# Kernel optimization log

Measured on AMD Instinct MI355X. Metric: run time of the kernel, lower is better.

The kernel has to match this reference:

```python
import jax, jax.numpy as jnp
import numpy as np

NI = 2048           # per-node feature dim
H = 2 * NI          # flattened per-sample GRU state (2 nodes)
BS = 4096
NO = 1
NUM_ROUNDS = 2


def setup_inputs() -> dict:
    key = jax.random.key(0)
    ks = jax.random.split(key, 8)
    s_ih = 1.0 / np.sqrt(H)
    features = jax.random.normal(ks[0], (BS, 2, NI), dtype=jnp.float32)
    # torch.nn.GRUCell(H, H): weight_ih [3H, H], weight_hh [3H, H], biases [3H]
    W_ih = jax.random.uniform(ks[1], (3 * H, H), minval=-s_ih, maxval=s_ih, dtype=jnp.float32)
    b_ih = jax.random.uniform(ks[2], (3 * H,), minval=-s_ih, maxval=s_ih, dtype=jnp.float32)
    W_hh = jax.random.uniform(ks[3], (3 * H, H), minval=-s_ih, maxval=s_ih, dtype=jnp.float32)
    b_hh = jax.random.uniform(ks[4], (3 * H,), minval=-s_ih, maxval=s_ih, dtype=jnp.float32)
    # fc = nn.Linear(2*ni, no)
    fc_w = jax.random.uniform(ks[5], (NO, H), minval=-s_ih, maxval=s_ih, dtype=jnp.float32)
    fc_b = jax.random.uniform(ks[6], (NO,), minval=-s_ih, maxval=s_ih, dtype=jnp.float32)
    return {"features": features, "W_ih": W_ih, "b_ih": b_ih,
            "W_hh": W_hh, "b_hh": b_hh, "fc_w": fc_w, "fc_b": fc_b}


def _gru_cell(x, h, W_ih, b_ih, W_hh, b_hh):
    # torch GRUCell semantics
    gi = x @ W_ih.T + b_ih              # [bs, 3H]
    gh = h @ W_hh.T + b_hh              # [bs, 3H]
    i_r, i_z, i_n = jnp.split(gi, 3, axis=-1)
    h_r, h_z, h_n = jnp.split(gh, 3, axis=-1)
    r = jax.nn.sigmoid(i_r + h_r)
    z = jax.nn.sigmoid(i_z + h_z)
    n = jnp.tanh(i_n + r * h_n)
    return (1.0 - z) * n + z * h


def reference(features, W_ih, b_ih, W_hh, b_hh, fc_w, fc_b):
    bs = features.shape[0]
    ni = features.shape[2]
    h = features.reshape(bs, -1)        # [bs, 2*ni] = node0 || node1
    for _ in range(NUM_ROUNDS):
        # fully-connected 2-node graph, sum-aggregate of neighbor messages:
        # node0 receives h1, node1 receives h0 -> x is the half-swap of h
        x = jnp.concatenate([h[:, ni:], h[:, :ni]], axis=-1)
        h = _gru_cell(x, h, W_ih, b_ih, W_hh, b_hh)
    return h @ fc_w.T + fc_b            # [bs, no]
```

## Files before the change

### kernel.cpp

```cpp
#include <hip/hip_runtime.h>


typedef __bf16 bf16x8 __attribute__((ext_vector_type(8)));
typedef float  f32x4  __attribute__((ext_vector_type(4)));
typedef unsigned short u16x4 __attribute__((ext_vector_type(4)));

#define HH    4096
#define NI_D  2048
#define N3H   12288
#define N6H   24576
#define BSZ   4096
#define BM    256
#define BN    256
#define BK    64
#define MT    (BSZ / BM)
#define NT    (N6H / BN)
#define GRID_GEMM (MT * NT)
#define NKT   (HH / BK)

__device__ __forceinline__ unsigned short f2bf(float f) {
  unsigned u = __float_as_uint(f);
  u += 0x7FFFu + ((u >> 16) & 1u);
  return (unsigned short)(u >> 16);
}
__device__ __forceinline__ float bf2f(unsigned short s) {
  return __uint_as_float(((unsigned)s) << 16);
}

__device__ __forceinline__ void gload16(const void* g, void* l) {
  void* gv = (void*)g;
  __builtin_amdgcn_global_load_lds(
      (__attribute__((address_space(1))) unsigned int*)gv,
      (__attribute__((address_space(3))) unsigned int*)l,
      16, 0, 0);
}

__global__ void __launch_bounds__(256)
convert_weights(const float* __restrict__ Wih, const float* __restrict__ Whh,
                unsigned short* __restrict__ Wc)
{
  int idx = (blockIdx.x * 256 + threadIdx.x) << 2;
  int j = idx >> 12;
  int k = idx & 4095;
  const float* src;
  if (j < N3H) src = Wih + (size_t)j * HH + ((k + NI_D) & (HH - 1));
  else         src = Whh + (size_t)(j - N3H) * HH + k;
  f32x4 v = *(const f32x4*)src;
  u16x4 o = { f2bf(v[0]), f2bf(v[1]), f2bf(v[2]), f2bf(v[3]) };
  *(u16x4*)(Wc + idx) = o;
}

__global__ void __launch_bounds__(256)
cast_f32_bf16(const float* __restrict__ src, unsigned short* __restrict__ dst)
{
  int i = (blockIdx.x * 256 + threadIdx.x) << 2;
  f32x4 v = *(const f32x4*)(src + i);
  u16x4 o = { f2bf(v[0]), f2bf(v[1]), f2bf(v[2]), f2bf(v[3]) };
  *(u16x4*)(dst + i) = o;
}

__global__ void __launch_bounds__(512, 2)
gemm_bt(const unsigned short* __restrict__ A,
        const unsigned short* __restrict__ B,
        unsigned short* __restrict__ C)
{
  __shared__ alignas(16) char ldsb[131072];

  int bid = blockIdx.x;
  int wg  = (bid & 7) * (GRID_GEMM / 8) + (bid >> 3);
  int nt  = wg / MT;
  int mt  = wg % MT;
  int m0  = mt * BM;
  int n0  = nt * BN;

  int t  = threadIdx.x;
  int wv = t >> 6;
  int l  = t & 63;
  int wm = wv >> 2;
  int wn = wv & 3;

  int srow  = wv * 8 + (l >> 3);
  int lbyte = ((l & 7) ^ (l >> 3)) << 4;
  unsigned aoff4[4], boff4[4];
#pragma unroll
  for (int r = 0; r < 4; ++r) {
    aoff4[r] = (unsigned)(m0 + r * 64 + srow) * (HH * 2) + lbyte;
    boff4[r] = (unsigned)(n0 + r * 64 + srow) * (HH * 2) + lbyte;
  }
  const char* Ab = (const char*)A;
  const char* Bb = (const char*)B;

  int offk0 = (((l >> 4) * 16))      ^ ((l & 7) << 4);
  int offk1 = (((l >> 4) * 16) + 64) ^ ((l & 7) << 4);
  int arow_off = (wm * 128 + (l & 15)) * 128;
  int brow_off = (wn * 64  + (l & 15)) * 128;

  f32x4 acc[8][4] = {};

#define STAGE(buf, kt) do {                                                   \
    int kk_ = ((kt) < NKT) ? (kt) : 0;                                        \
    unsigned kb_ = (unsigned)kk_ * 128;                                       \
    _Pragma("unroll")                                                         \
    for (int r_ = 0; r_ < 4; ++r_) {                                          \
      gload16(Ab + (size_t)(aoff4[r_] + kb_),                                 \
              ldsb + (buf) * 32768 + r_ * 8192 + wv * 1024);                  \
      gload16(Bb + (size_t)(boff4[r_] + kb_),                                 \
              ldsb + 65536 + (buf) * 32768 + r_ * 8192 + wv * 1024);          \
    }                                                                         \
  } while (0)

#define TILE(buf, ktn) do {                                                   \
    asm volatile("s_waitcnt vmcnt(8)" ::: "memory");                          \
    __builtin_amdgcn_s_barrier();                                             \
    asm volatile("" ::: "memory");                                            \
    const char* LA_ = ldsb + (buf) * 32768 + arow_off;                        \
    const char* LB_ = ldsb + 65536 + (buf) * 32768 + brow_off;                \
    bf16x8 bfr[4][2];                                                         \
    _Pragma("unroll")                                                         \
    for (int nf_ = 0; nf_ < 4; ++nf_) {                                       \
      bfr[nf_][0] = *(const bf16x8*)(LB_ + nf_ * 2048 + offk0);               \
      bfr[nf_][1] = *(const bf16x8*)(LB_ + nf_ * 2048 + offk1);               \
    }                                                                         \
    _Pragma("unroll")                                                         \
    for (int qm_ = 0; qm_ < 2; ++qm_) {                                       \
      bf16x8 afr[4][2];                                                       \
      _Pragma("unroll")                                                       \
      for (int m_ = 0; m_ < 4; ++m_) {                                        \
        afr[m_][0] = *(const bf16x8*)(LA_ + (qm_ * 4 + m_) * 2048 + offk0);   \
        afr[m_][1] = *(const bf16x8*)(LA_ + (qm_ * 4 + m_) * 2048 + offk1);   \
      }                                                                       \
      __builtin_amdgcn_s_setprio(1);                                          \
      _Pragma("unroll")                                                       \
      for (int ks_ = 0; ks_ < 2; ++ks_)                                       \
        _Pragma("unroll")                                                     \
        for (int m_ = 0; m_ < 4; ++m_)                                        \
          _Pragma("unroll")                                                   \
          for (int nf_ = 0; nf_ < 4; ++nf_)                                   \
            acc[qm_ * 4 + m_][nf_] = __builtin_amdgcn_mfma_f32_16x16x32_bf16( \
                afr[m_][ks_], bfr[nf_][ks_], acc[qm_ * 4 + m_][nf_], 0, 0, 0);\
      __builtin_amdgcn_s_setprio(0);                                          \
    }                                                                         \
    asm volatile("" ::: "memory");                                            \
    __builtin_amdgcn_s_barrier();                                             \
    STAGE(buf, ktn);                                                          \
  } while (0)

  STAGE(0, 0);
  STAGE(1, 1);
#pragma unroll 1
  for (int tt = 0; tt < NKT; tt += 2) {
    TILE(0, tt + 2);
    TILE(1, tt + 3);
  }
  asm volatile("s_waitcnt vmcnt(0)" ::: "memory");

#undef TILE
#undef STAGE

  int crow = m0 + wm * 128 + ((l >> 4) << 2);
  int ccol = n0 + wn * 64 + (l & 15);
#pragma unroll
  for (int mf = 0; mf < 8; ++mf)
#pragma unroll
    for (int nf = 0; nf < 4; ++nf)
#pragma unroll
      for (int i = 0; i < 4; ++i)
        C[(size_t)(crow + mf * 16 + i) * N6H + (ccol + nf * 16)] =
            f2bf(acc[mf][nf][i]);
}

__global__ void __launch_bounds__(256)
gru_update(const unsigned short* __restrict__ C, const float* __restrict__ h_old,
           const float* __restrict__ b_ih, const float* __restrict__ b_hh,
           float* __restrict__ h_new, unsigned short* __restrict__ h_bf)
{
  int idx = blockIdx.x * 256 + threadIdx.x;
  int b = idx >> 10;
  int j = (idx & 1023) << 2;
  const unsigned short* Cr = C + (size_t)b * N6H;
  u16x4 gir = *(const u16x4*)(Cr + j);
  u16x4 giz = *(const u16x4*)(Cr + HH + j);
  u16x4 gin = *(const u16x4*)(Cr + 2 * HH + j);
  u16x4 ghr = *(const u16x4*)(Cr + 3 * HH + j);
  u16x4 ghz = *(const u16x4*)(Cr + 4 * HH + j);
  u16x4 ghn = *(const u16x4*)(Cr + 5 * HH + j);
  f32x4 bir = *(const f32x4*)(b_ih + j);
  f32x4 biz = *(const f32x4*)(b_ih + HH + j);
  f32x4 bin = *(const f32x4*)(b_ih + 2 * HH + j);
  f32x4 bhr = *(const f32x4*)(b_hh + j);
  f32x4 bhz = *(const f32x4*)(b_hh + HH + j);
  f32x4 bhn = *(const f32x4*)(b_hh + 2 * HH + j);
  f32x4 ho  = *(const f32x4*)(h_old + (size_t)b * HH + j);
  f32x4 hv; u16x4 hb;
#pragma unroll
  for (int e = 0; e < 4; ++e) {
    float r = 1.f / (1.f + expf(-(bf2f(gir[e]) + bir[e] + bf2f(ghr[e]) + bhr[e])));
    float z = 1.f / (1.f + expf(-(bf2f(giz[e]) + biz[e] + bf2f(ghz[e]) + bhz[e])));
    float n = tanhf(bf2f(gin[e]) + bin[e] + r * (bf2f(ghn[e]) + bhn[e]));
    float h = (1.f - z) * n + z * ho[e];
    hv[e] = h; hb[e] = f2bf(h);
  }
  *(f32x4*)(h_new + (size_t)b * HH + j) = hv;
  *(u16x4*)(h_bf + (size_t)b * HH + j)  = hb;
}

__global__ void __launch_bounds__(256)
final_fc(const float* __restrict__ h, const float* __restrict__ fcw,
         const float* __restrict__ fcb, float* __restrict__ out)
{
  int b = blockIdx.x, t = threadIdx.x;
  const float* row = h + (size_t)b * HH;
  float s = 0.f;
#pragma unroll
  for (int i = 0; i < 4; ++i) {
    int v4 = t + i * 256;
    f32x4 hv = *(const f32x4*)(row + v4 * 4);
    f32x4 wv = *(const f32x4*)(fcw + v4 * 4);
    s += hv[0] * wv[0] + hv[1] * wv[1] + hv[2] * wv[2] + hv[3] * wv[3];
  }
#pragma unroll
  for (int off = 32; off > 0; off >>= 1) s += __shfl_down(s, off);
  __shared__ float red[4];
  if ((t & 63) == 0) red[t >> 6] = s;
  __syncthreads();
  if (t == 0) out[b] = red[0] + red[1] + red[2] + red[3] + fcb[0];
}

extern "C" void kernel_launch(void* const* d_in, const int* in_sizes, int n_in,
                              void* d_out, int out_size, void* d_ws, size_t ws_size,
                              hipStream_t stream)
{
  const float* feat = (const float*)d_in[0];
  const float* Wih  = (const float*)d_in[1];
  const float* bih  = (const float*)d_in[2];
  const float* Whh  = (const float*)d_in[3];
  const float* bhh  = (const float*)d_in[4];
  const float* fcw  = (const float*)d_in[5];
  const float* fcb  = (const float*)d_in[6];
  float* out = (float*)d_out;

  char* ws = (char*)d_ws;
  unsigned short* Wc   = (unsigned short*)ws;
  unsigned short* Cbuf = (unsigned short*)(ws + 201326592);
  unsigned short* hb   = (unsigned short*)(ws + 402653184);
  float*          hf   = (float*)(ws + 436207616);

  convert_weights<<<98304, 256, 0, stream>>>(Wih, Whh, Wc);
  cast_f32_bf16<<<16384, 256, 0, stream>>>(feat, hb);

  gemm_bt<<<GRID_GEMM, 512, 0, stream>>>(hb, Wc, Cbuf);
  gru_update<<<16384, 256, 0, stream>>>(Cbuf, feat, bih, bhh, hf, hb);

  gemm_bt<<<GRID_GEMM, 512, 0, stream>>>(hb, Wc, Cbuf);
  gru_update<<<16384, 256, 0, stream>>>(Cbuf, hf, bih, bhh, hf, hb);

  final_fc<<<4096, 256, 0, stream>>>(hf, fcw, fcb, out);
}
```

Baseline: 1.756 ms.

## Interleave global-to-LDS staging with MFMA sub-blocks in GEMM k-loop

```diff
diff --git a/kernel.cpp b/kernel.cpp
--- a/kernel.cpp
+++ b/kernel.cpp
@@ -59,12 +59,112 @@
   *(u16x4*)(dst + i) = o;
 }
 
+__device__ __forceinline__ void stageA(const char* a_base, char* lds, int ldst,
+                                       int d, int kt, int g) {
+  int kc = (kt < NKT) ? kt : 0;
+  gload16(a_base + (size_t)kc * 128 + (size_t)g * 524288,
+          lds + d * 32768 + g * 8192 + ldst);
+}
+__device__ __forceinline__ void stageB(const char* b_base, char* lds, int ldst,
+                                       int d, int kt, int g) {
+  int kc = (kt < NKT) ? kt : 0;
+  gload16(b_base + (size_t)kc * 128 + (size_t)g * 524288,
+          lds + 65536 + d * 32768 + g * 8192 + ldst);
+}
+
+template <int MB>
+__device__ __forceinline__ void mfma16(f32x4 (&acc)[8][4],
+                                       const bf16x8 (&aA)[2], const bf16x8 (&aB)[2],
+                                       const bf16x8 (&bfr)[4][2]) {
+  __builtin_amdgcn_s_setprio(1);
+#pragma unroll
+  for (int ks = 0; ks < 2; ++ks)
+#pragma unroll
+    for (int nf = 0; nf < 4; ++nf) {
+      acc[MB][nf]     = __builtin_amdgcn_mfma_f32_16x16x32_bf16(
+                          aA[ks], bfr[nf][ks], acc[MB][nf], 0, 0, 0);
+      acc[MB + 1][nf] = __builtin_amdgcn_mfma_f32_16x16x32_bf16(
+                          aB[ks], bfr[nf][ks], acc[MB + 1][nf], 0, 0, 0);
+    }
+  __builtin_amdgcn_s_setprio(0);
+}
+
+#define BAR   __builtin_amdgcn_s_barrier()
+#define LGKM0 do { asm volatile("s_waitcnt lgkmcnt(0)" ::: "memory");          \
+                   __builtin_amdgcn_sched_barrier(0); } while (0)
+
+template <int D>
+__device__ __forceinline__ void kblock(char* lds, const char* a_base,
+                                       const char* b_base, int ldst,
+                                       int aro, int bro, int offk0, int offk1,
+                                       int t1, int t2, f32x4 (&acc)[8][4]) {
+  const char* LA = lds + D * 32768 + aro;
+  const char* LB = lds + 65536 + D * 32768 + bro;
+  bf16x8 bfr[4][2];
+
+  {
+#pragma unroll
+    for (int nf = 0; nf < 4; ++nf) {
+      bfr[nf][0] = *(const bf16x8*)(LB + nf * 2048 + offk0);
+      bfr[nf][1] = *(const bf16x8*)(LB + nf * 2048 + offk1);
+    }
+    bf16x8 aA[2], aB[2];
+    aA[0] = *(const bf16x8*)(LA + 6 * 2048 + offk0);
+    aA[1] = *(const bf16x8*)(LA + 6 * 2048 + offk1);
+    aB[0] = *(const bf16x8*)(LA + 7 * 2048 + offk0);
+    aB[1] = *(const bf16x8*)(LA + 7 * 2048 + offk1);
+    stageA(a_base, lds, ldst, D ^ 1, t1, 0);
+    stageA(a_base, lds, ldst, D ^ 1, t1, 2);
+    asm volatile("s_waitcnt lgkmcnt(8)" ::: "memory");
+    BAR; LGKM0;
+    mfma16<6>(acc, aA, aB, bfr);
+    BAR;
+  }
+  {
+    bf16x8 aA[2], aB[2];
+    aA[0] = *(const bf16x8*)(LA + 4 * 2048 + offk0);
+    aA[1] = *(const bf16x8*)(LA + 4 * 2048 + offk1);
+    aB[0] = *(const bf16x8*)(LA + 5 * 2048 + offk0);
+    aB[1] = *(const bf16x8*)(LA + 5 * 2048 + offk1);
+    stageB(b_base, lds, ldst, D, t2, 0);
+    stageB(b_base, lds, ldst, D, t2, 1);
+    BAR; LGKM0;
+    mfma16<4>(acc, aA, aB, bfr);
+    BAR;
+  }
+  {
+    bf16x8 aA[2], aB[2];
+    aA[0] = *(const bf16x8*)(LA + 2 * 2048 + offk0);
+    aA[1] = *(const bf16x8*)(LA + 2 * 2048 + offk1);
+    aB[0] = *(const bf16x8*)(LA + 3 * 2048 + offk0);
+    aB[1] = *(const bf16x8*)(LA + 3 * 2048 + offk1);
+    stageB(b_base, lds, ldst, D, t2, 2);
+    stageB(b_base, lds, ldst, D, t2, 3);
+    BAR; LGKM0;
+    mfma16<2>(acc, aA, aB, bfr);
+    BAR;
+  }
+  {
+    bf16x8 aA[2], aB[2];
+    aA[0] = *(const bf16x8*)(LA + 0 * 2048 + offk0);
+    aA[1] = *(const bf16x8*)(LA + 0 * 2048 + offk1);
+    aB[0] = *(const bf16x8*)(LA + 1 * 2048 + offk0);
+    aB[1] = *(const bf16x8*)(LA + 1 * 2048 + offk1);
+    stageA(a_base, lds, ldst, D, t2, 1);
+    stageA(a_base, lds, ldst, D, t2, 3);
+    BAR; LGKM0;
+    mfma16<0>(acc, aA, aB, bfr);
+    asm volatile("s_waitcnt vmcnt(6)" ::: "memory");
+    BAR;
+  }
+}
+
 __global__ void __launch_bounds__(512, 2)
 gemm_bt(const unsigned short* __restrict__ A,
         const unsigned short* __restrict__ B,
         unsigned short* __restrict__ C)
 {
-  __shared__ alignas(16) char ldsb[131072];
+  __shared__ alignas(16) char lds[131072];
 
   int bid = blockIdx.x;
   int wg  = (bid & 7) * (GRID_GEMM / 8) + (bid >> 3);
@@ -79,83 +179,38 @@
   int wm = wv >> 2;
   int wn = wv & 3;
 
-  int srow  = wv * 8 + (l >> 3);
-  int lbyte = ((l & 7) ^ (l >> 3)) << 4;
-  unsigned aoff4[4], boff4[4];
-#pragma unroll
-  for (int r = 0; r < 4; ++r) {
-    aoff4[r] = (unsigned)(m0 + r * 64 + srow) * (HH * 2) + lbyte;
-    boff4[r] = (unsigned)(n0 + r * 64 + srow) * (HH * 2) + lbyte;
-  }
-  const char* Ab = (const char*)A;
-  const char* Bb = (const char*)B;
-
-  int offk0 = (((l >> 4) * 16))      ^ ((l & 7) << 4);
-  int offk1 = (((l >> 4) * 16) + 64) ^ ((l & 7) << 4);
-  int arow_off = (wm * 128 + (l & 15)) * 128;
-  int brow_off = (wn * 64  + (l & 15)) * 128;
+  int rloc   = wv * 8 + (l >> 3);
+  int sg_col = ((l & 7) ^ (l >> 3)) << 4;
+  const char* a_base = (const char*)A + (size_t)(m0 + rloc) * 8192 + sg_col;
+  const char* b_base = (const char*)B + (size_t)(n0 + rloc) * 8192 + sg_col;
+  int ldst = wv * 1024;
+
+  int offk0 = (((l >> 4) << 4)) ^ ((l & 7) << 4);
+  int offk1 = offk0 ^ 64;
+  int aro = (wm * 128 + (l & 15)) * 128;
+  int bro = (wn * 64  + (l & 15)) * 128;
 
   f32x4 acc[8][4] = {};
 
-#define STAGE(buf, kt) do {                                                   \
-    int kk_ = ((kt) < NKT) ? (kt) : 0;                                        \
-    unsigned kb_ = (unsigned)kk_ * 128;                                       \
-    _Pragma("unroll")                                                         \
-    for (int r_ = 0; r_ < 4; ++r_) {                                          \
-      gload16(Ab + (size_t)(aoff4[r_] + kb_),                                 \
-              ldsb + (buf) * 32768 + r_ * 8192 + wv * 1024);                  \
-      gload16(Bb + (size_t)(boff4[r_] + kb_),                                 \
-              ldsb + 65536 + (buf) * 32768 + r_ * 8192 + wv * 1024);          \
-    }                                                                         \
-  } while (0)
-
-#define TILE(buf, ktn) do {                                                   \
-    asm volatile("s_waitcnt vmcnt(8)" ::: "memory");                          \
-    __builtin_amdgcn_s_barrier();                                             \
-    asm volatile("" ::: "memory");                                            \
-    const char* LA_ = ldsb + (buf) * 32768 + arow_off;                        \
-    const char* LB_ = ldsb + 65536 + (buf) * 32768 + brow_off;                \
-    bf16x8 bfr[4][2];                                                         \
-    _Pragma("unroll")                                                         \
-    for (int nf_ = 0; nf_ < 4; ++nf_) {                                       \
-      bfr[nf_][0] = *(const bf16x8*)(LB_ + nf_ * 2048 + offk0);               \
-      bfr[nf_][1] = *(const bf16x8*)(LB_ + nf_ * 2048 + offk1);               \
-    }                                                                         \
-    _Pragma("unroll")                                                         \
-    for (int qm_ = 0; qm_ < 2; ++qm_) {                                       \
-      bf16x8 afr[4][2];                                                       \
-      _Pragma("unroll")                                                       \
-      for (int m_ = 0; m_ < 4; ++m_) {                                        \
-        afr[m_][0] = *(const bf16x8*)(LA_ + (qm_ * 4 + m_) * 2048 + offk0);   \
-        afr[m_][1] = *(const bf16x8*)(LA_ + (qm_ * 4 + m_) * 2048 + offk1);   \
-      }                                                                       \
-      __builtin_amdgcn_s_setprio(1);                                          \
-      _Pragma("unroll")                                                       \
-      for (int ks_ = 0; ks_ < 2; ++ks_)                                       \
-        _Pragma("unroll")                                                     \
-        for (int m_ = 0; m_ < 4; ++m_)                                        \
-          _Pragma("unroll")                                                   \
-          for (int nf_ = 0; nf_ < 4; ++nf_)                                   \
-            acc[qm_ * 4 + m_][nf_] = __builtin_amdgcn_mfma_f32_16x16x32_bf16( \
-                afr[m_][ks_], bfr[nf_][ks_], acc[qm_ * 4 + m_][nf_], 0, 0, 0);\
-      __builtin_amdgcn_s_setprio(0);                                          \
-    }                                                                         \
-    asm volatile("" ::: "memory");                                            \
-    __builtin_amdgcn_s_barrier();                                             \
-    STAGE(buf, ktn);                                                          \
-  } while (0)
-
-  STAGE(0, 0);
-  STAGE(1, 1);
+#pragma unroll
+  for (int g = 0; g < 4; ++g) stageA(a_base, lds, ldst, 0, 0, g);
+#pragma unroll
+  for (int g = 0; g < 4; ++g) stageB(b_base, lds, ldst, 0, 0, g);
+#pragma unroll
+  for (int g = 0; g < 4; ++g) stageB(b_base, lds, ldst, 1, 1, g);
+  stageA(a_base, lds, ldst, 1, 1, 1);
+  stageA(a_base, lds, ldst, 1, 1, 3);
+  asm volatile("s_waitcnt vmcnt(6)" ::: "memory");
+  BAR;
+
 #pragma unroll 1
   for (int tt = 0; tt < NKT; tt += 2) {
-    TILE(0, tt + 2);
-    TILE(1, tt + 3);
+    kblock<0>(lds, a_base, b_base, ldst, aro, bro, offk0, offk1,
+              tt + 1, tt + 2, acc);
+    kblock<1>(lds, a_base, b_base, ldst, aro, bro, offk0, offk1,
+              tt + 2, tt + 3, acc);
   }
   asm volatile("s_waitcnt vmcnt(0)" ::: "memory");
-
-#undef TILE
-#undef STAGE
 
   int crow = m0 + wm * 128 + ((l >> 4) << 2);
   int ccol = n0 + wn * 64 + (l & 15);
```

Result: faster. 1.570 ms (-10.6%).
